# Kernel optimization log

Hardware: AMD Instinct MI355X
Metric: run time of the kernel (lower is better)

Reference implementation:

```python
import jax, jax.numpy as jnp
import numpy as np

N_HEADS = 4
TEMPERATURE = 1.0
EPS = 1e-10
LN_EPS = 1e-5


def _l2norm(t):
    # matches kernel: t / sqrt(sum(t*t) + 1e-10)
    return t / jnp.sqrt(jnp.sum(t * t, axis=-1, keepdims=True) + EPS)


def setup_inputs() -> dict:
    key = jax.random.key(0)
    ks = jax.random.split(key, 12)
    N, S, L = 2048, 1024, 2048
    s = 0.02
    return {
        "x": jax.random.normal(ks[0], (N, S), dtype=jnp.float32),
        "We": jax.random.normal(ks[1], (S, L), dtype=jnp.float32) * s,
        "be": jnp.zeros((L,), dtype=jnp.float32),
        "Wq": jax.random.normal(ks[2], (S, L), dtype=jnp.float32) * s,
        "bq": jnp.zeros((L,), dtype=jnp.float32),
        "Wk": jax.random.normal(ks[3], (L, L), dtype=jnp.float32) * s,
        "bk": jnp.zeros((L,), dtype=jnp.float32),
        "Wv": jax.random.normal(ks[4], (L, L), dtype=jnp.float32) * s,
        "bv": jnp.zeros((L,), dtype=jnp.float32),
        "ln_g": jnp.ones((L,), dtype=jnp.float32),
        "ln_b": jnp.zeros((L,), dtype=jnp.float32),
        "Wd": jax.random.normal(ks[5], (L, S), dtype=jnp.float32) * s,
        "bd": jnp.zeros((S,), dtype=jnp.float32),
    }


def reference(x, We, be, Wq, bq, Wk, bk, Wv, bv, ln_g, ln_b, Wd, bd):
    N, L = x.shape[0], We.shape[1]
    P = N_HEADS
    d = L // P
    # encode (sensory -> latent), tanh
    h = jnp.tanh(x @ We + be)                      # [N, L]
    # projections: query from sensory input, key/value from latent
    q = (x @ Wq + bq).reshape(N, P, d).transpose(1, 0, 2)   # [P, N, d]
    k = (h @ Wk + bk).reshape(N, P, d).transpose(1, 0, 2)
    v = (h @ Wv + bv).reshape(N, P, d).transpose(1, 0, 2)
    # cosine-normalized attention with metabolic temperature (attention_kernel)
    qn = _l2norm(q)
    kn = _l2norm(k)
    scale = 1.0 / ((float(d) ** 0.5) * TEMPERATURE)
    scores = jnp.einsum('pnd,pmd->pnm', qn, kn) * scale      # [P, N, N]
    m = jnp.max(scores, axis=-1, keepdims=True)
    p = jnp.exp(scores - m)
    attn = jnp.einsum('pnm,pmd->pnd', p, v) / (jnp.sum(p, axis=-1, keepdims=True) + EPS)
    a = attn.transpose(1, 0, 2).reshape(N, L)                # concat heads
    # LayerNorm
    mu = jnp.mean(a, axis=-1, keepdims=True)
    var = jnp.mean((a - mu) ** 2, axis=-1, keepdims=True)
    y = ln_g * (a - mu) / jnp.sqrt(var + LN_EPS) + ln_b
    out = jnp.tanh(y @ Wd + bd)                              # decode
    # pseudopod correlation kernel: row-L2-normalized k @ v^T per head
    corr = jnp.einsum('pnd,pmd->pnm', kn, _l2norm(v))        # [P, N, N]
    return out, corr
```

## Files before the change

kernel.cpp:

```cpp
#include <hip/hip_runtime.h>
#include <cmath>
#include <cstdint>


typedef __attribute__((ext_vector_type(8))) _Float16 half8;
typedef __attribute__((ext_vector_type(4))) float f32x4;

typedef __attribute__((address_space(1))) void GV;
typedef __attribute__((address_space(3))) void LV;

__device__ __forceinline__ void load_lds16(const _Float16* g, _Float16* l) {
  __builtin_amdgcn_global_load_lds((GV*)g, (LV*)l, 16, 0, 0);
}

template <int EPI, int BM, int BN>
__global__ __launch_bounds__(256) void gemm_nt(
    const _Float16* __restrict__ A, const _Float16* __restrict__ B,
    void* __restrict__ Cv, int K, int lda, int ldb, int ldc,
    long aZ, long bZ, long cZ,
    const float* __restrict__ bias0, const float* __restrict__ bias1,
    float scale, const float* __restrict__ rowIn,
    const float* __restrict__ colIn, float* __restrict__ redOut) {
  constexpr int MR = BM / 32, NR = BN / 32;
  __shared__ _Float16 As[2][BM * 32];
  __shared__ _Float16 Bs[2][BN * 32];

  const int z = blockIdx.z;
  A += (long)z * aZ;
  B += (long)z * bZ;

  const int tid = threadIdx.x;
  const int wave = tid >> 6;
  const int lane = tid & 63;
  const int brow = blockIdx.y * BM;
  const int bcol = blockIdx.x * BN;
  const int wr = (wave >> 1) * (BM / 2);
  const int wc = (wave & 1) * (BN / 2);

  const int srow = tid >> 2;
  const int sslot = (tid & 3) ^ ((srow >> 1) & 3);
  const int scol = sslot * 8;
  const _Float16* ga = A + (long)(brow + srow) * lda + scol;
  const _Float16* gb = B + (long)(bcol + srow) * ldb + scol;
  const long a64 = (long)64 * lda;
  const long b64 = (long)64 * ldb;
  const int lofs = wave * 512;

  f32x4 acc[MR][NR];
#pragma unroll
  for (int m = 0; m < MR; ++m)
#pragma unroll
    for (int n = 0; n < NR; ++n) acc[m][n] = f32x4{0.f, 0.f, 0.f, 0.f};

  const int fr = lane & 15;
  const int fkx = (((lane >> 4) ^ ((fr >> 1) & 3))) * 8;
  const int nt = K >> 5;

  load_lds16(ga, &As[0][lofs]);
  if constexpr (BM == 128) load_lds16(ga + a64, &As[0][2048 + lofs]);
  load_lds16(gb, &Bs[0][lofs]);
  if constexpr (BN == 128) load_lds16(gb + b64, &Bs[0][2048 + lofs]);

  for (int t = 0; t < nt; ++t) {
    const int cur = t & 1;
    __syncthreads();
    if (t + 1 < nt) {
      const int ko = (t + 1) << 5;
      const int nb = cur ^ 1;
      load_lds16(ga + ko, &As[nb][lofs]);
      if constexpr (BM == 128) load_lds16(ga + ko + a64, &As[nb][2048 + lofs]);
      load_lds16(gb + ko, &Bs[nb][lofs]);
      if constexpr (BN == 128) load_lds16(gb + ko + b64, &Bs[nb][2048 + lofs]);
    }
    half8 af[MR], bf[NR];
#pragma unroll
    for (int m = 0; m < MR; ++m)
      af[m] = *(const half8*)&As[cur][(wr + m * 16 + fr) * 32 + fkx];
#pragma unroll
    for (int n = 0; n < NR; ++n)
      bf[n] = *(const half8*)&Bs[cur][(wc + n * 16 + fr) * 32 + fkx];
#pragma unroll
    for (int m = 0; m < MR; ++m)
#pragma unroll
      for (int n = 0; n < NR; ++n)
        acc[m][n] = __builtin_amdgcn_mfma_f32_16x16x32_f16(af[m], bf[n],
                                                           acc[m][n], 0, 0, 0);
  }

  const int r0 = (lane >> 4) * 4;

  if constexpr (EPI == 0 || EPI == 1) {
    const float* bs = (z == 0) ? bias0 : bias1;
    _Float16* C = (_Float16*)Cv + (long)z * cZ;
    float ss[MR][4];
#pragma unroll
    for (int m = 0; m < MR; ++m)
#pragma unroll
      for (int r = 0; r < 4; ++r) ss[m][r] = 0.f;
#pragma unroll
    for (int m = 0; m < MR; ++m)
#pragma unroll
      for (int n = 0; n < NR; ++n) {
        const int col = bcol + wc + n * 16 + fr;
        const float bv = bs[col];
#pragma unroll
        for (int r = 0; r < 4; ++r) {
          const int row = brow + wr + m * 16 + r0 + r;
          const float val = acc[m][n][r] + bv;
          if (EPI == 0 && z == 0) {
            C[(long)row * ldc + col] = (_Float16)tanhf(val);
          } else {
            C[(long)row * ldc + col] = (_Float16)val;
            ss[m][r] += val * val;
          }
        }
      }
    if (EPI == 1 || z == 1) {
      const int head = (bcol + wc) >> 9;
      float* sq = redOut + (EPI == 1 ? z * 8192 : 0) + head * 2048;
#pragma unroll
      for (int m = 0; m < MR; ++m)
#pragma unroll
        for (int r = 0; r < 4; ++r) {
          float s = ss[m][r];
          s += __shfl_xor(s, 1);
          s += __shfl_xor(s, 2);
          s += __shfl_xor(s, 4);
          s += __shfl_xor(s, 8);
          if (fr == 0) atomicAdd(&sq[brow + wr + m * 16 + r0 + r], s);
        }
    }
  } else if constexpr (EPI == 2) {
    _Float16* C = (_Float16*)Cv + (long)z * cZ;
    const float* sA = rowIn + z * 2048;
    const float* sB = colIn + z * 2048;
    float rj[NR];
#pragma unroll
    for (int n = 0; n < NR; ++n)
      rj[n] = rsqrtf(sB[bcol + wc + n * 16 + fr] + 1e-10f);
    float rowacc[MR][4];
#pragma unroll
    for (int m = 0; m < MR; ++m)
#pragma unroll
      for (int r = 0; r < 4; ++r) {
        const int row = brow + wr + m * 16 + r0 + r;
        const float ri = rsqrtf(sA[row] + 1e-10f) * scale;
        float ra = 0.f;
#pragma unroll
        for (int n = 0; n < NR; ++n) {
          const int col = bcol + wc + n * 16 + fr;
          const float val = expf(acc[m][n][r] * ri * rj[n]);
          C[(long)row * ldc + col] = (_Float16)val;
          ra += val;
        }
        rowacc[m][r] = ra;
      }
    float* rs = redOut + z * 2048;
#pragma unroll
    for (int m = 0; m < MR; ++m)
#pragma unroll
      for (int r = 0; r < 4; ++r) {
        float s = rowacc[m][r];
        s += __shfl_xor(s, 1);
        s += __shfl_xor(s, 2);
        s += __shfl_xor(s, 4);
        s += __shfl_xor(s, 8);
        if (fr == 0) atomicAdd(&rs[brow + wr + m * 16 + r0 + r], s);
      }
  } else if constexpr (EPI == 3) {
    float* C = (float*)Cv + (long)z * cZ;
    const float* rs = rowIn + z * 2048;
#pragma unroll
    for (int m = 0; m < MR; ++m)
#pragma unroll
      for (int r = 0; r < 4; ++r) {
        const int row = brow + wr + m * 16 + r0 + r;
        const float inv = 1.f / (rs[row] + 1e-10f);
#pragma unroll
        for (int n = 0; n < NR; ++n) {
          const int col = bcol + wc + n * 16 + fr;
          C[(long)row * ldc + col] = acc[m][n][r] * inv;
        }
      }
  } else if constexpr (EPI == 4) {
    float* C = (float*)Cv;
#pragma unroll
    for (int m = 0; m < MR; ++m)
#pragma unroll
      for (int n = 0; n < NR; ++n) {
        const int col = bcol + wc + n * 16 + fr;
        const float bv = bias0[col];
#pragma unroll
        for (int r = 0; r < 4; ++r) {
          const int row = brow + wr + m * 16 + r0 + r;
          C[(long)row * ldc + col] = tanhf(acc[m][n][r] + bv);
        }
      }
  } else if constexpr (EPI == 5) {
    float* C = (float*)Cv + (long)z * cZ;
    const float* sA = rowIn + z * 2048;
    const float* sB = colIn + z * 2048;
    float rj[NR];
#pragma unroll
    for (int n = 0; n < NR; ++n)
      rj[n] = rsqrtf(sB[bcol + wc + n * 16 + fr] + 1e-10f);
#pragma unroll
    for (int m = 0; m < MR; ++m)
#pragma unroll
      for (int r = 0; r < 4; ++r) {
        const int row = brow + wr + m * 16 + r0 + r;
        const float ri = rsqrtf(sA[row] + 1e-10f);
#pragma unroll
        for (int n = 0; n < NR; ++n) {
          const int col = bcol + wc + n * 16 + fr;
          C[(long)row * ldc + col] = acc[m][n][r] * ri * rj[n];
        }
      }
  }
}


__global__ __launch_bounds__(256) void cvt_f32_f16(const float* __restrict__ s,
                                                   _Float16* __restrict__ d,
                                                   long n) {
  const long i = ((long)blockIdx.x * 256 + threadIdx.x) * 8;
  if (i + 8 > n) return;
  const float4 a = *(const float4*)(s + i);
  const float4 b = *(const float4*)(s + i + 4);
  half8 o;
  o[0] = (_Float16)a.x; o[1] = (_Float16)a.y; o[2] = (_Float16)a.z; o[3] = (_Float16)a.w;
  o[4] = (_Float16)b.x; o[5] = (_Float16)b.y; o[6] = (_Float16)b.z; o[7] = (_Float16)b.w;
  *(half8*)(d + i) = o;
}

__global__ __launch_bounds__(256) void transpose_cast2(
    const float* __restrict__ s0, const float* __restrict__ s1,
    _Float16* __restrict__ d, int R, int C) {
  __shared__ float tile[32][33];
  const float* src = blockIdx.z ? s1 : s0;
  _Float16* dst = d + (size_t)blockIdx.z * R * C;
  const int bx = blockIdx.x * 32, by = blockIdx.y * 32;
  const int tx = threadIdx.x & 31, ty = threadIdx.x >> 5;
#pragma unroll
  for (int i = 0; i < 32; i += 8)
    tile[ty + i][tx] = src[(long)(by + ty + i) * C + bx + tx];
  __syncthreads();
#pragma unroll
  for (int i = 0; i < 32; i += 8)
    dst[(long)(bx + ty + i) * R + by + tx] = (_Float16)tile[tx][ty + i];
}

__global__ __launch_bounds__(256) void transpose_f16(
    const _Float16* __restrict__ src, _Float16* __restrict__ dst, int R, int C) {
  __shared__ _Float16 tile[32][33];
  const int bx = blockIdx.x * 32, by = blockIdx.y * 32;
  const int tx = threadIdx.x & 31, ty = threadIdx.x >> 5;
#pragma unroll
  for (int i = 0; i < 32; i += 8)
    tile[ty + i][tx] = src[(long)(by + ty + i) * C + bx + tx];
  __syncthreads();
#pragma unroll
  for (int i = 0; i < 32; i += 8)
    dst[(long)(bx + ty + i) * R + by + tx] = tile[tx][ty + i];
}

__global__ __launch_bounds__(256) void layernorm_f16(
    const float* __restrict__ a, const float* __restrict__ g,
    const float* __restrict__ b, _Float16* __restrict__ y) {
  const long row = blockIdx.x;
  const float* src = a + row * 2048;
  const int t = threadIdx.x, lane = t & 63, wv = t >> 6;
  const float4 v0 = *(const float4*)(src + t * 8);
  const float4 v1 = *(const float4*)(src + t * 8 + 4);
  float vals[8] = {v0.x, v0.y, v0.z, v0.w, v1.x, v1.y, v1.z, v1.w};
  float s = 0.f;
#pragma unroll
  for (int i = 0; i < 8; ++i) s += vals[i];
#pragma unroll
  for (int off = 1; off < 64; off <<= 1) s += __shfl_xor(s, off);
  __shared__ float sr1[4], sr2[4];
  if (lane == 0) sr1[wv] = s;
  __syncthreads();
  const float mu = (sr1[0] + sr1[1] + sr1[2] + sr1[3]) * (1.f / 2048.f);
  float d2 = 0.f;
#pragma unroll
  for (int i = 0; i < 8; ++i) {
    const float dd = vals[i] - mu;
    d2 += dd * dd;
  }
#pragma unroll
  for (int off = 1; off < 64; off <<= 1) d2 += __shfl_xor(d2, off);
  if (lane == 0) sr2[wv] = d2;
  __syncthreads();
  const float var = (sr2[0] + sr2[1] + sr2[2] + sr2[3]) * (1.f / 2048.f);
  const float inv = rsqrtf(var + 1e-5f);
#pragma unroll
  for (int i = 0; i < 8; ++i) {
    const int col = t * 8 + i;
    y[row * 2048 + col] = (_Float16)(g[col] * (vals[i] - mu) * inv + b[col]);
  }
}


extern "C" void kernel_launch(void* const* d_in, const int* in_sizes, int n_in,
                              void* d_out, int out_size, void* d_ws,
                              size_t ws_size, hipStream_t stream) {
  (void)in_sizes; (void)n_in; (void)out_size; (void)ws_size;
  const float* x = (const float*)d_in[0];
  const float* We = (const float*)d_in[1];
  const float* be = (const float*)d_in[2];
  const float* Wq = (const float*)d_in[3];
  const float* bq = (const float*)d_in[4];
  const float* Wk = (const float*)d_in[5];
  const float* bk = (const float*)d_in[6];
  const float* Wv = (const float*)d_in[7];
  const float* bv = (const float*)d_in[8];
  const float* lng = (const float*)d_in[9];
  const float* lnb = (const float*)d_in[10];
  const float* Wd = (const float*)d_in[11];
  const float* bd = (const float*)d_in[12];

  float* out = (float*)d_out;
  float* corr = out + (size_t)2048 * 1024;

  char* w = (char*)d_ws;
  auto alloc = [&](size_t nbytes) -> void* {
    void* p = (void*)w;
    w += (nbytes + 255) & ~(size_t)255;
    return p;
  };
  const long NN = (long)2048 * 2048;
  _Float16* xh  = (_Float16*)alloc((size_t)2048 * 1024 * 2);
  _Float16* WeT = (_Float16*)alloc((size_t)2048 * 1024 * 2);
  _Float16* WqT = (_Float16*)alloc((size_t)2048 * 1024 * 2);
  _Float16* WkT = (_Float16*)alloc((size_t)2048 * 2048 * 2);
  _Float16* WvT = (_Float16*)alloc((size_t)2048 * 2048 * 2);
  _Float16* WdT = (_Float16*)alloc((size_t)1024 * 2048 * 2);
  _Float16* hh  = (_Float16*)alloc((size_t)NN * 2);
  _Float16* qh  = (_Float16*)alloc((size_t)NN * 2);
  _Float16* kh  = (_Float16*)alloc((size_t)NN * 2);
  _Float16* vh  = (_Float16*)alloc((size_t)NN * 2);
  _Float16* vT  = (_Float16*)alloc((size_t)NN * 2);
  _Float16* ph  = (_Float16*)alloc((size_t)4 * NN * 2);
  float* stats  = (float*)alloc((size_t)4 * 8192 * 4);
  float* af     = (float*)alloc((size_t)NN * 4);
  _Float16* yh  = (_Float16*)alloc((size_t)NN * 2);
  float* sqQ = stats;
  float* sqK = stats + 8192;
  float* sqV = stats + 16384;
  float* rsum = stats + 24576;

  const dim3 blk(256);

  cvt_f32_f16<<<dim3(1024), blk, 0, stream>>>(x, xh, (long)2048 * 1024);
  transpose_cast2<<<dim3(64, 32, 2), blk, 0, stream>>>(We, Wq, WeT, 1024, 2048);
  transpose_cast2<<<dim3(64, 64, 2), blk, 0, stream>>>(Wk, Wv, WkT, 2048, 2048);
  transpose_cast2<<<dim3(32, 64, 1), blk, 0, stream>>>(Wd, Wd, WdT, 2048, 1024);
  hipMemsetAsync(stats, 0, (size_t)4 * 8192 * 4, stream);

  gemm_nt<0, 128, 64><<<dim3(32, 16, 2), blk, 0, stream>>>(
      xh, WeT, hh, 1024, 1024, 1024, 2048, 0L, (long)2048 * 1024, NN,
      be, bq, 0.f, nullptr, nullptr, sqQ);
  gemm_nt<1, 128, 64><<<dim3(32, 16, 2), blk, 0, stream>>>(
      hh, WkT, kh, 2048, 2048, 2048, 2048, 0L, (long)2048 * 2048, NN,
      bk, bv, 0.f, nullptr, nullptr, sqK);
  transpose_f16<<<dim3(64, 64), blk, 0, stream>>>(vh, vT, 2048, 2048);
  const float scl = 1.0f / sqrtf(512.f);
  gemm_nt<2, 128, 128><<<dim3(16, 16, 4), blk, 0, stream>>>(
      qh, kh, ph, 512, 2048, 2048, 2048, 512L, 512L, NN,
      nullptr, nullptr, scl, sqQ, sqK, rsum);
  gemm_nt<3, 64, 64><<<dim3(8, 32, 4), blk, 0, stream>>>(
      ph, vT, af, 2048, 2048, 2048, 2048, NN, (long)512 * 2048, 512L,
      nullptr, nullptr, 0.f, rsum, nullptr, nullptr);
  layernorm_f16<<<dim3(2048), blk, 0, stream>>>(af, lng, lnb, yh);
  gemm_nt<4, 64, 64><<<dim3(16, 32, 1), blk, 0, stream>>>(
      yh, WdT, out, 2048, 2048, 2048, 1024, 0L, 0L, 0L,
      bd, nullptr, 0.f, nullptr, nullptr, nullptr);
  gemm_nt<5, 128, 128><<<dim3(16, 16, 4), blk, 0, stream>>>(
      kh, vh, corr, 512, 2048, 2048, 2048, 512L, 512L, NN,
      nullptr, nullptr, 0.f, sqK, sqV, nullptr);
}
```

Baseline: 408.8 us.

## Triple-buffer GEMM LDS tiles with explicit vmcnt waits and raw barriers

Moves the shared GEMM main loop from double to triple buffering of A/B tiles, prefetching two K-steps ahead via direct global-to-LDS loads. It replaces __syncthreads with a partial s_waitcnt vmcnt plus s_barrier so only the oldest stage must land before compute, and issues the next prefetch after fragments are read. This aims to hide global load latency better, at the cost of 50% more LDS, which may reduce occupancy, and reliance on exact vmcnt counting for correctness.

```diff
diff --git a/kernel.cpp b/kernel.cpp
--- a/kernel.cpp
+++ b/kernel.cpp
@@ -11,6 +11,14 @@
 
 __device__ __forceinline__ void load_lds16(const _Float16* g, _Float16* l) {
   __builtin_amdgcn_global_load_lds((GV*)g, (LV*)l, 16, 0, 0);
+}
+
+template <int N>
+__device__ __forceinline__ void wait_vmcnt() {
+  asm volatile("s_waitcnt vmcnt(%0)" ::"n"(N) : "memory");
+}
+__device__ __forceinline__ void hw_barrier() {
+  asm volatile("s_barrier" ::: "memory");
 }
 
 template <int EPI, int BM, int BN>
@@ -22,8 +30,9 @@
     float scale, const float* __restrict__ rowIn,
     const float* __restrict__ colIn, float* __restrict__ redOut) {
   constexpr int MR = BM / 32, NR = BN / 32;
-  __shared__ _Float16 As[2][BM * 32];
-  __shared__ _Float16 Bs[2][BN * 32];
+  constexpr int LPT = (BM == 128 ? 2 : 1) + (BN == 128 ? 2 : 1);
+  __shared__ _Float16 As[3][BM * 32];
+  __shared__ _Float16 Bs[3][BN * 32];
 
   const int z = blockIdx.z;
   A += (long)z * aZ;
@@ -46,6 +55,14 @@
   const long b64 = (long)64 * ldb;
   const int lofs = wave * 512;
 
+  auto stage = [&](int t, int b) {
+    const int ko = t << 5;
+    load_lds16(ga + ko, &As[b][lofs]);
+    if constexpr (BM == 128) load_lds16(ga + ko + a64, &As[b][2048 + lofs]);
+    load_lds16(gb + ko, &Bs[b][lofs]);
+    if constexpr (BN == 128) load_lds16(gb + ko + b64, &Bs[b][2048 + lofs]);
+  };
+
   f32x4 acc[MR][NR];
 #pragma unroll
   for (int m = 0; m < MR; ++m)
@@ -56,22 +73,34 @@
   const int fkx = (((lane >> 4) ^ ((fr >> 1) & 3))) * 8;
   const int nt = K >> 5;
 
-  load_lds16(ga, &As[0][lofs]);
-  if constexpr (BM == 128) load_lds16(ga + a64, &As[0][2048 + lofs]);
-  load_lds16(gb, &Bs[0][lofs]);
-  if constexpr (BN == 128) load_lds16(gb + b64, &Bs[0][2048 + lofs]);
-
-  for (int t = 0; t < nt; ++t) {
-    const int cur = t & 1;
-    __syncthreads();
-    if (t + 1 < nt) {
-      const int ko = (t + 1) << 5;
-      const int nb = cur ^ 1;
-      load_lds16(ga + ko, &As[nb][lofs]);
-      if constexpr (BM == 128) load_lds16(ga + ko + a64, &As[nb][2048 + lofs]);
-      load_lds16(gb + ko, &Bs[nb][lofs]);
-      if constexpr (BN == 128) load_lds16(gb + ko + b64, &Bs[nb][2048 + lofs]);
-    }
+  stage(0, 0);
+  stage(1, 1);
+
+  int cur = 0, nxt2 = 2;
+  for (int t = 0; t < nt - 1; ++t) {
+    wait_vmcnt<LPT>();
+    hw_barrier();
+    half8 af[MR], bf[NR];
+#pragma unroll
+    for (int m = 0; m < MR; ++m)
+      af[m] = *(const half8*)&As[cur][(wr + m * 16 + fr) * 32 + fkx];
+#pragma unroll
+    for (int n = 0; n < NR; ++n)
+      bf[n] = *(const half8*)&Bs[cur][(wc + n * 16 + fr) * 32 + fkx];
+    if (t + 2 < nt) stage(t + 2, nxt2);
+#pragma unroll
+    for (int m = 0; m < MR; ++m)
+#pragma unroll
+      for (int n = 0; n < NR; ++n)
+        acc[m][n] = __builtin_amdgcn_mfma_f32_16x16x32_f16(af[m], bf[n],
+                                                           acc[m][n], 0, 0, 0);
+    __builtin_amdgcn_sched_barrier(0);
+    cur = (cur == 2) ? 0 : cur + 1;
+    nxt2 = (nxt2 == 2) ? 0 : nxt2 + 1;
+  }
+  wait_vmcnt<0>();
+  hw_barrier();
+  {
     half8 af[MR], bf[NR];
 #pragma unroll
     for (int m = 0; m < MR; ++m)
```

Result: no change. 407.4 us (-0.3%).
